# Kernel optimization log

Measured on AMD Instinct MI355X. Metric: run time of the kernel, lower is better.

## Reference

```python
import jax, jax.numpy as jnp
import numpy as np

THRESHOLD = 0.3

def setup_inputs() -> dict:
    key = jax.random.key(0)
    ks = jax.random.split(key, 8)
    B, T, N, d = 4, 32, 1024, 2
    hd, od, hs, osz = 64, 64, 128, 2
    p = lambda k, sh: jax.random.normal(k, sh, jnp.float32) * 0.1
    return {
        "points": jax.random.uniform(ks[0], (B, T, N, d), jnp.float32),
        "W1": p(ks[1], (hd, d)),   "b1": jnp.zeros((hd,), jnp.float32),
        "W2": p(ks[2], (od, hd)),  "b2": jnp.zeros((od,), jnp.float32),
        "Wg": p(ks[3], (hd, od)),  "bg": jnp.zeros((hd,), jnp.float32),
        "Wih": p(ks[4], (3 * hs, hd)), "Whh": p(ks[5], (3 * hs, hs)),
        "bih": jnp.zeros((3 * hs,), jnp.float32), "bhh": jnp.zeros((3 * hs,), jnp.float32),
        "Wf": p(ks[6], (osz, hs)), "bf": jnp.zeros((osz,), jnp.float32),
    }

def _gcn_step(pts, W1, b1, W2, b2, Wg, bg):
    # pts: [N, d]. Torch detaches node features & adjacency (no grad to points).
    pts = jax.lax.stop_gradient(pts)
    dist = jnp.linalg.norm(pts[:, None, :] - pts[None, :, :], axis=2)  # [N,N]
    A = (dist < THRESHOLD).astype(pts.dtype)
    dinv = 1.0 / jnp.sqrt(A.sum(axis=1))          # rowsum >= 1 (self-loop)
    An = A * dinv[:, None] * dinv[None, :]        # D^{-1/2} A D^{-1/2}
    x = jax.nn.relu((An @ pts) @ W1.T + b1)       # [N, hd]
    x = jax.nn.relu((An @ x) @ W2.T + b2)         # [N, od]
    return x.mean(axis=0) @ Wg.T + bg             # [hd]

def reference(points, W1, b1, W2, b2, Wg, bg, Wih, Whh, bih, bhh, Wf, bf):
    # GCN per (batch, time): [B, T, hd]
    gcn = jax.vmap(jax.vmap(lambda p: _gcn_step(p, W1, b1, W2, b2, Wg, bg)))(points)
    H = Whh.shape[1]

    def gru_step(h, x):  # torch GRU gate order: r, z, n
        gi = x @ Wih.T + bih
        gh = h @ Whh.T + bhh
        ir, iz, inn = jnp.split(gi, 3)
        hr, hz, hn = jnp.split(gh, 3)
        r = jax.nn.sigmoid(ir + hr)
        z = jax.nn.sigmoid(iz + hz)
        n = jnp.tanh(inn + r * hn)
        h_new = (1.0 - z) * n + z * h
        return h_new, h_new

    h0 = jnp.zeros((H,), points.dtype)
    run = lambda xs: jax.lax.scan(gru_step, h0, xs)[1]   # [T, H]
    hs = jax.vmap(run)(gcn)                              # [B, T, H]
    y = hs @ Wf.T + bf                                   # [B, T, out]
    # torch: per-element gru_out.mean(dim=1, keepdim=True) on [1,T,out] -> [1,1,out], stacked -> [B,1,1,out]
    return y.mean(axis=1, keepdims=True)[:, :, None, :]
```

## Files before the change

kernel.cpp:

```cpp
#include <hip/hip_runtime.h>
#include <hip/hip_bf16.h>
#include <math.h>

#define N_PTS 1024
#define BT    128
typedef unsigned int u32;
typedef __attribute__((ext_vector_type(8))) short short8_t;
typedef __attribute__((ext_vector_type(4))) float f32x4;

__device__ __forceinline__ float bfi(u32 bits16) {
    union { u32 u; float f; } v; v.u = bits16 << 16; return v.f;
}
__device__ __forceinline__ unsigned short f2bf(float f) {
    union { float f; u32 u; } v; v.f = f;
    return (unsigned short)((v.u + 0x7FFFu + ((v.u >> 16) & 1u)) >> 16);
}
__device__ __forceinline__ float ldf(const void* p, int i, bool bf) {
    return bf ? bfi(((const unsigned short*)p)[i]) : ((const float*)p)[i];
}
__device__ __forceinline__ float2 ldp(const void* pbase, int j, bool bf) {
    if (bf) {
        u32 w = ((const u32*)pbase)[j];
        return make_float2(bfi(w & 0xFFFFu), bfi(w >> 16));
    }
    return ((const float2*)pbase)[j];
}
__device__ __forceinline__ bool detect_bf16(const void* pts, int tid, int* s_flag) {
    if (tid < 64) {
        u32 w = ((const u32*)pts)[tid];
        float v = bfi(w & 0xFFFFu);
        bool ok = (v >= 0.0f) && (v <= 1.0f);
        unsigned long long m = __ballot(ok);
        if (tid == 0) *s_flag = (m == 0xFFFFFFFFFFFFFFFFull) ? 1 : 0;
    }
    __syncthreads();
    return *s_flag != 0;
}
__device__ __forceinline__ bool is_nb(float px, float py, float qx, float qy) {
    float dx = px - qx, dy = py - qy;
    float d2 = __fadd_rn(__fmul_rn(dx, dx), __fmul_rn(dy, dy));
    return d2 < 0.09f;
}
__device__ __forceinline__ const void* pts_base(const void* pts, int bt, bool bf) {
    return bf ? (const void*)((const unsigned short*)pts + (size_t)bt * N_PTS * 2)
              : (const void*)((const float*)pts + (size_t)bt * N_PTS * 2);
}
__device__ __forceinline__ void gload16(const u32* g, u32* l) {
    __builtin_amdgcn_global_load_lds((const __attribute__((address_space(1))) u32*)g,
                                     (__attribute__((address_space(3))) u32*)l, 16, 0, 0);
}

__global__ __launch_bounds__(256) void k1_bm(const void* __restrict__ pts,
                                             float* __restrict__ dinv,
                                             float* __restrict__ gsum,
                                             u32* __restrict__ bm) {
    int blk = blockIdx.x, tid = threadIdx.x;
    int bt = blk >> 2, q = blk & 3;
    __shared__ float2 sp[N_PTS];
    __shared__ int s_flag;
    bool bf = detect_bf16(pts, tid, &s_flag);
    const void* pb = pts_base(pts, bt, bf);
    for (int j = tid; j < N_PTS; j += 256) sp[j] = ldp(pb, j, bf);
    if (blk < 32) gsum[blk * 256 + tid] = 0.0f;
    __syncthreads();
    int i = q * 256 + tid;
    float px = sp[i].x, py = sp[i].y;
    const float4* sp4 = (const float4*)sp;
    u32* bmrow = bm + (size_t)bt * 32768 + i;
    int cnt = 0;
    for (int c = 0; c < 32; c++) {
        u32 m = 0;
#pragma unroll
        for (int h = 0; h < 8; h++) {
            float4 s01 = sp4[c * 16 + 2 * h], s23 = sp4[c * 16 + 2 * h + 1];
            if (is_nb(px, py, s01.x, s01.y)) m |= 1u << (4 * h);
            if (is_nb(px, py, s01.z, s01.w)) m |= 1u << (4 * h + 1);
            if (is_nb(px, py, s23.x, s23.y)) m |= 1u << (4 * h + 2);
            if (is_nb(px, py, s23.z, s23.w)) m |= 1u << (4 * h + 3);
        }
        bmrow[c * 1024] = m;
        cnt += __popc(m);
    }
    dinv[bt * N_PTS + i] = 1.0f / sqrtf((float)cnt);
}

__global__ __launch_bounds__(256) void k2_x1v(const void* __restrict__ pts,
                                              const void* __restrict__ W1,
                                              const void* __restrict__ b1,
                                              const float* __restrict__ dinv,
                                              const u32* __restrict__ bm,
                                              u32* __restrict__ x1vB) {
    int blk = blockIdx.x, tid = threadIdx.x;
    int bt = blk >> 2, q = blk & 3;
    __shared__ float2 sud[N_PTS];
    __shared__ float2 sax[256];
    __shared__ float  sdl[256];
    __shared__ int s_flag;
    bool bf = detect_bf16(pts, tid, &s_flag);
    const void* pb = pts_base(pts, bt, bf);
    for (int j = tid; j < N_PTS; j += 256) {
        float2 p = ldp(pb, j, bf);
        float d = dinv[bt * N_PTS + j];
        sud[j] = make_float2(d * p.x, d * p.y);
    }
    __syncthreads();
    int i = q * 256 + tid;
    float ax = 0.f, ay = 0.f;
    const u32* bmr = bm + (size_t)bt * 32768 + i;
    for (int c = 0; c < 32; c++) {
        u32 m = bmr[c * 1024];
        const float4* uv = (const float4*)sud + c * 16;
#pragma unroll
        for (int h = 0; h < 16; h++) {
            float4 v = uv[h];
            bool b0 = (m >> (2 * h)) & 1u, b1_ = (m >> (2 * h + 1)) & 1u;
            ax += b0 ? v.x : 0.0f;  ay += b0 ? v.y : 0.0f;
            ax += b1_ ? v.z : 0.0f; ay += b1_ ? v.w : 0.0f;
        }
    }
    float di = dinv[bt * N_PTS + i];
    sax[tid] = make_float2(ax * di, ay * di);
    sdl[tid] = di;
    __syncthreads();
    int ch = tid & 63, wq = tid >> 6;
    float w0 = ldf(W1, 2 * ch, bf), w1v = ldf(W1, 2 * ch + 1, bf), bb = ldf(b1, ch, bf);
    for (int tt = 0; tt < 4; tt++) {
        u32 ow[8];
#pragma unroll
        for (int k2i = 0; k2i < 8; k2i++) {
            int lj = tt * 64 + wq * 16 + 2 * k2i;
            float2 a0 = sax[lj], a1 = sax[lj + 1];
            float v0 = sdl[lj]     * fmaxf(fmaf(w0, a0.x, fmaf(w1v, a0.y, bb)), 0.0f);
            float v1 = sdl[lj + 1] * fmaxf(fmaf(w0, a1.x, fmaf(w1v, a1.y, bb)), 0.0f);
            ow[k2i] = (u32)f2bf(v0) | ((u32)f2bf(v1) << 16);
        }
        u32* dst = x1vB + ((size_t)(bt * 16 + q * 4 + tt) * 64 + ch) * 36 + wq * 8;
        *(uint4*)dst = make_uint4(ow[0], ow[1], ow[2], ow[3]);
        *(uint4*)(dst + 4) = make_uint4(ow[4], ow[5], ow[6], ow[7]);
    }
}

__global__ __launch_bounds__(256) void k3_mfma(const void* __restrict__ pts,
                                               const void* __restrict__ W2,
                                               const void* __restrict__ b2,
                                               const float* __restrict__ dinv,
                                               const u32* __restrict__ bm,
                                               const u32* __restrict__ x1vB,
                                               float* __restrict__ gsum) {
    __shared__ u32 pool[15424];
    __shared__ int s_flag;
    float* poolf = (float*)pool;
    int tid = threadIdx.x, lane = tid & 63, w = tid >> 6;
    int l15 = lane & 15, quad = lane >> 4;
    int blk = blockIdx.x, bt = blk & 127, rowblk = blk >> 7;
    bool bf = detect_bf16(pts, tid, &s_flag);

    const u32* xg = x1vB + (size_t)bt * 36864;
    for (int it = w; it < 9; it += 4)
        gload16(xg + it * 256 + lane * 4, pool + 8192 + it * 256 + lane * 4);

    const u32* bg_ = bm + (size_t)bt * 32768 + rowblk * 256;
    for (int idx = tid; idx < 8192; idx += 256) {
        int c = idx >> 8, r = idx & 255;
        pool[idx] = bg_[c * 1024 + r];
    }
    unsigned short* W2B = (unsigned short*)(pool + 12800);
    for (int idx = tid; idx < 4096; idx += 256) {
        int o = idx >> 6, c = idx & 63;
        W2B[o * 72 + c] = f2bf(ldf(W2, idx, bf));
    }
    if (tid < 256) poolf[15104 + tid] = dinv[bt * N_PTS + rowblk * 256 + tid];
    if (tid < 64)  poolf[15360 + tid] = ldf(b2, tid, bf);

    f32x4 acc[4][4];
#pragma unroll
    for (int rf = 0; rf < 4; rf++)
#pragma unroll
        for (int nb = 0; nb < 4; nb++)
#pragma unroll
            for (int r = 0; r < 4; r++) acc[rf][nb][r] = 0.0f;

    for (int t = 0; t < 16; t++) {
        __syncthreads();
        if (t + 1 < 16) {
            u32* dst = pool + ((t & 1) ? 8192 : 10496);
            const u32* src = xg + (t + 1) * 2304;
            for (int it = w; it < 9; it += 4)
                gload16(src + it * 256 + lane * 4, dst + it * 256 + lane * 4);
        }
        const unsigned short* xf = (const unsigned short*)(pool + ((t & 1) ? 10496 : 8192));
#pragma unroll
        for (int ks = 0; ks < 2; ks++) {
            short8_t bq[4];
#pragma unroll
            for (int rf = 0; rf < 4; rf++) {
                u32 mw = pool[(2 * t + ks) * 256 + w * 64 + rf * 16 + l15];
                u32 by = (mw >> (quad * 8)) & 0xFFu;
                short8_t v;
#pragma unroll
                for (int i2 = 0; i2 < 8; i2++)
                    v[i2] = (by & (1u << i2)) ? (short)0x3F80 : (short)0;
                bq[rf] = v;
            }
#pragma unroll
            for (int nb = 0; nb < 4; nb++) {
                short8_t af = *(const short8_t*)(xf + (nb * 16 + l15) * 72 + ks * 32 + quad * 8);
#pragma unroll
                for (int rf = 0; rf < 4; rf++)
                    acc[rf][nb] = __builtin_amdgcn_mfma_f32_16x16x32_bf16(af, bq[rf], acc[rf][nb], 0, 0, 0);
            }
        }
    }
    __syncthreads();

    u32* dump = pool;
#pragma unroll
    for (int rf = 0; rf < 4; rf++) {
        int rn = w * 64 + rf * 16 + l15;
        float di = poolf[15104 + rn];
#pragma unroll
        for (int nb = 0; nb < 4; nb++) {
            u32 lo = (u32)f2bf(acc[rf][nb][0] * di) | ((u32)f2bf(acc[rf][nb][1] * di) << 16);
            u32 hi = (u32)f2bf(acc[rf][nb][2] * di) | ((u32)f2bf(acc[rf][nb][3] * di) << 16);
            u32* dst = dump + rn * 36 + nb * 8 + quad * 2;
            dst[0] = lo; dst[1] = hi;
        }
    }
    __syncthreads();
    f32x4 xacc[4][4];
#pragma unroll
    for (int ob = 0; ob < 4; ob++)
#pragma unroll
        for (int rf = 0; rf < 4; rf++)
#pragma unroll
            for (int r = 0; r < 4; r++) xacc[ob][rf][r] = 0.0f;
#pragma unroll
    for (int ks2 = 0; ks2 < 2; ks2++) {
        short8_t b2f[4];
#pragma unroll
        for (int rf = 0; rf < 4; rf++)
            b2f[rf] = *(const short8_t*)((const unsigned short*)dump +
                        (w * 64 + rf * 16 + l15) * 72 + ks2 * 32 + quad * 8);
#pragma unroll
        for (int ob = 0; ob < 4; ob++) {
            short8_t a2 = *(const short8_t*)(W2B + (ob * 16 + l15) * 72 + ks2 * 32 + quad * 8);
#pragma unroll
            for (int rf = 0; rf < 4; rf++)
                xacc[ob][rf] = __builtin_amdgcn_mfma_f32_16x16x32_bf16(a2, b2f[rf], xacc[ob][rf], 0, 0, 0);
        }
    }
#pragma unroll
    for (int ob = 0; ob < 4; ob++) {
#pragma unroll
        for (int r = 0; r < 4; r++) {
            int o = ob * 16 + quad * 4 + r;
            float bb = poolf[15360 + o];
            float s = 0.0f;
#pragma unroll
            for (int rf = 0; rf < 4; rf++) s += fmaxf(xacc[ob][rf][r] + bb, 0.0f);
            s += __shfl_down(s, 8, 16);
            s += __shfl_down(s, 4, 16);
            s += __shfl_down(s, 2, 16);
            s += __shfl_down(s, 1, 16);
            if (l15 == 0) atomicAdd(&gsum[bt * 64 + o], s);
        }
    }
}

__global__ __launch_bounds__(384) void k4_all(const void* __restrict__ pts,
                                              const void* __restrict__ Wg,
                                              const void* __restrict__ bg,
                                              const void* __restrict__ Wih,
                                              const void* __restrict__ Whh,
                                              const void* __restrict__ bih,
                                              const void* __restrict__ bhh,
                                              const void* __restrict__ Wf,
                                              const void* __restrict__ bf_,
                                              const float* __restrict__ gsum,
                                              float* __restrict__ out) {
    int b = blockIdx.x, tid = threadIdx.x;
    __shared__ float s_gi[32 * 384];
    __shared__ float sWgT[64 * 65];
    __shared__ float s_gm[2048];
    __shared__ float s_x[2048];
    __shared__ float s_gh[384];
    __shared__ float s_h[128];
    __shared__ float s_hsum[128];
    __shared__ int s_flag;
    bool bf = detect_bf16(pts, tid, &s_flag);
    for (int idx = tid; idx < 4096; idx += 384) {
        int o = idx >> 6, k = idx & 63;
        sWgT[k * 65 + o] = ldf(Wg, idx, bf);
    }
    for (int idx = tid; idx < 2048; idx += 384)
        s_gm[idx] = gsum[(size_t)b * 2048 + idx] * (1.0f / 1024.0f);
    if (tid < 128) { s_h[tid] = 0.0f; s_hsum[tid] = 0.0f; }
    __syncthreads();
    for (int idx = tid; idx < 2048; idx += 384) {
        int t = idx >> 6, c = idx & 63;
        float s = ldf(bg, c, bf);
        for (int k = 0; k < 64; k++) s = fmaf(sWgT[k * 65 + c], s_gm[t * 64 + k], s);
        s_x[idx] = s;
    }
    __syncthreads();
    {
        int r = tid;
        float wv[64];
        if (bf) {
#pragma unroll
            for (int k = 0; k < 64; k++) wv[k] = bfi(((const unsigned short*)Wih)[r * 64 + k]);
        } else {
            const float4* wr = (const float4*)Wih + r * 16;
#pragma unroll
            for (int qq = 0; qq < 16; qq++) {
                float4 v = wr[qq];
                wv[4*qq] = v.x; wv[4*qq+1] = v.y; wv[4*qq+2] = v.z; wv[4*qq+3] = v.w;
            }
        }
        float br = ldf(bih, r, bf);
        for (int t = 0; t < 32; t++) {
            float s = br;
#pragma unroll
            for (int k = 0; k < 64; k++) s = fmaf(wv[k], s_x[t * 64 + k], s);
            s_gi[t * 384 + r] = s;
        }
    }
    float wh[128];
    if (bf) {
#pragma unroll
        for (int k = 0; k < 128; k++) wh[k] = bfi(((const unsigned short*)Whh)[tid * 128 + k]);
    } else {
        const float4* wr = (const float4*)Whh + tid * 32;
#pragma unroll
        for (int qq = 0; qq < 32; qq++) {
            float4 v = wr[qq];
            wh[4*qq] = v.x; wh[4*qq+1] = v.y; wh[4*qq+2] = v.z; wh[4*qq+3] = v.w;
        }
    }
    float bhr = ldf(bhh, tid, bf);
    __syncthreads();
    for (int t = 0; t < 32; t++) {
        float s = bhr;
#pragma unroll
        for (int k = 0; k < 128; k++) s = fmaf(wh[k], s_h[k], s);
        s_gh[tid] = s;
        __syncthreads();
        if (tid < 128) {
            int c = tid;
            float gr = s_gi[t * 384 + c]       + s_gh[c];
            float gz = s_gi[t * 384 + 128 + c] + s_gh[128 + c];
            float gn = s_gi[t * 384 + 256 + c];
            float hn = s_gh[256 + c];
            float r = 1.0f / (1.0f + expf(-gr));
            float z = 1.0f / (1.0f + expf(-gz));
            float n = tanhf(fmaf(r, hn, gn));
            float hnew = (1.0f - z) * n + z * s_h[c];
            s_h[c] = hnew;
            s_hsum[c] += hnew;
        }
        __syncthreads();
    }
    if (tid < 2) {
        float s = ldf(bf_, tid, bf);
        for (int k = 0; k < 128; k++)
            s = fmaf(ldf(Wf, tid * 128 + k, bf), s_hsum[k] * (1.0f / 32.0f), s);
        out[b * 2 + tid] = s;
    }
}

extern "C" void kernel_launch(void* const* d_in, const int* in_sizes, int n_in,
                              void* d_out, int out_size, void* d_ws, size_t ws_size,
                              hipStream_t stream) {
    const void* pts = d_in[0];
    const void* W1  = d_in[1];
    const void* b1  = d_in[2];
    const void* W2  = d_in[3];
    const void* b2  = d_in[4];
    const void* Wg  = d_in[5];
    const void* bg  = d_in[6];
    const void* Wih = d_in[7];
    const void* Whh = d_in[8];
    const void* bih = d_in[9];
    const void* bhh = d_in[10];
    const void* Wf  = d_in[11];
    const void* bf_ = d_in[12];

    float* dinv = (float*)d_ws;
    float* gsum = dinv + (size_t)BT * N_PTS;
    u32*   bm   = (u32*)(gsum + BT * 64);
    u32*   x1vB = bm + (size_t)BT * 32768;

    k1_bm  <<<512, 256, 0, stream>>>(pts, dinv, gsum, bm);
    k2_x1v <<<512, 256, 0, stream>>>(pts, W1, b1, dinv, bm, x1vB);
    k3_mfma<<<512, 256, 0, stream>>>(pts, W2, b2, dinv, bm, x1vB, gsum);
    k4_all <<<4, 384, 0, stream>>>(pts, Wg, bg, Wih, Whh, bih, bhh, Wf, bf_,
                                   gsum, (float*)d_out);
}
```

Baseline: 251.4 us.

## Split GRU recurrence matvec across 768 threads with K-halved partial sums

Doubles the GRU kernel's block size to 768 threads. Each half of the block computes the hidden-to-hidden matvec over half of the K dimension, and the two partial results are summed in shared memory, which shortens the serial 32-step recurrence chain. The input projection and Wg projections also use multiple independent accumulators with float4 shared loads, and the hidden state is kept in a register. The cost is more threads per block, each holding 64 weight registers, plus an extra partial-sum read per gate.

```diff
diff --git a/kernel.cpp b/kernel.cpp
--- a/kernel.cpp
+++ b/kernel.cpp
@@ -267,44 +267,51 @@
     }
 }
 
-__global__ __launch_bounds__(384) void k4_all(const void* __restrict__ pts,
-                                              const void* __restrict__ Wg,
-                                              const void* __restrict__ bg,
-                                              const void* __restrict__ Wih,
-                                              const void* __restrict__ Whh,
-                                              const void* __restrict__ bih,
-                                              const void* __restrict__ bhh,
-                                              const void* __restrict__ Wf,
-                                              const void* __restrict__ bf_,
-                                              const float* __restrict__ gsum,
-                                              float* __restrict__ out) {
+__global__ __launch_bounds__(768, 1) void k4_all(const void* __restrict__ pts,
+                                                 const void* __restrict__ Wg,
+                                                 const void* __restrict__ bg,
+                                                 const void* __restrict__ Wih,
+                                                 const void* __restrict__ Whh,
+                                                 const void* __restrict__ bih,
+                                                 const void* __restrict__ bhh,
+                                                 const void* __restrict__ Wf,
+                                                 const void* __restrict__ bf_,
+                                                 const float* __restrict__ gsum,
+                                                 float* __restrict__ out) {
     int b = blockIdx.x, tid = threadIdx.x;
     __shared__ float s_gi[32 * 384];
     __shared__ float sWgT[64 * 65];
     __shared__ float s_gm[2048];
     __shared__ float s_x[2048];
-    __shared__ float s_gh[384];
+    __shared__ float s_part[768];
     __shared__ float s_h[128];
-    __shared__ float s_hsum[128];
     __shared__ int s_flag;
     bool bf = detect_bf16(pts, tid, &s_flag);
-    for (int idx = tid; idx < 4096; idx += 384) {
+    for (int idx = tid; idx < 4096; idx += 768) {
         int o = idx >> 6, k = idx & 63;
         sWgT[k * 65 + o] = ldf(Wg, idx, bf);
     }
-    for (int idx = tid; idx < 2048; idx += 384)
+    for (int idx = tid; idx < 2048; idx += 768)
         s_gm[idx] = gsum[(size_t)b * 2048 + idx] * (1.0f / 1024.0f);
-    if (tid < 128) { s_h[tid] = 0.0f; s_hsum[tid] = 0.0f; }
-    __syncthreads();
-    for (int idx = tid; idx < 2048; idx += 384) {
+    if (tid < 128) s_h[tid] = 0.0f;
+    __syncthreads();
+    for (int idx = tid; idx < 2048; idx += 768) {
         int t = idx >> 6, c = idx & 63;
-        float s = ldf(bg, c, bf);
-        for (int k = 0; k < 64; k++) s = fmaf(sWgT[k * 65 + c], s_gm[t * 64 + k], s);
-        s_x[idx] = s;
-    }
-    __syncthreads();
+        float s0 = ldf(bg, c, bf), s1 = 0.f, s2 = 0.f, s3 = 0.f;
+        const float* gm = s_gm + t * 64;
+#pragma unroll
+        for (int k = 0; k < 64; k += 4) {
+            s0 = fmaf(sWgT[k * 65 + c],       gm[k],     s0);
+            s1 = fmaf(sWgT[(k + 1) * 65 + c], gm[k + 1], s1);
+            s2 = fmaf(sWgT[(k + 2) * 65 + c], gm[k + 2], s2);
+            s3 = fmaf(sWgT[(k + 3) * 65 + c], gm[k + 3], s3);
+        }
+        s_x[idx] = (s0 + s1) + (s2 + s3);
+    }
+    __syncthreads();
+    int hi = (tid >= 384) ? 1 : 0;
+    int r = tid - hi * 384;
     {
-        int r = tid;
         float wv[64];
         if (bf) {
 #pragma unroll
@@ -318,52 +325,76 @@
             }
         }
         float br = ldf(bih, r, bf);
-        for (int t = 0; t < 32; t++) {
-            float s = br;
-#pragma unroll
-            for (int k = 0; k < 64; k++) s = fmaf(wv[k], s_x[t * 64 + k], s);
-            s_gi[t * 384 + r] = s;
-        }
-    }
-    float wh[128];
-    if (bf) {
-#pragma unroll
-        for (int k = 0; k < 128; k++) wh[k] = bfi(((const unsigned short*)Whh)[tid * 128 + k]);
-    } else {
-        const float4* wr = (const float4*)Whh + tid * 32;
-#pragma unroll
-        for (int qq = 0; qq < 32; qq++) {
-            float4 v = wr[qq];
-            wh[4*qq] = v.x; wh[4*qq+1] = v.y; wh[4*qq+2] = v.z; wh[4*qq+3] = v.w;
-        }
-    }
-    float bhr = ldf(bhh, tid, bf);
-    __syncthreads();
+        for (int t = hi; t < 32; t += 2) {
+            float s0 = br, s1 = 0.f, s2 = 0.f, s3 = 0.f;
+            const float4* x4 = (const float4*)(s_x + t * 64);
+#pragma unroll
+            for (int qq = 0; qq < 16; qq++) {
+                float4 v = x4[qq];
+                s0 = fmaf(wv[4*qq],   v.x, s0);
+                s1 = fmaf(wv[4*qq+1], v.y, s1);
+                s2 = fmaf(wv[4*qq+2], v.z, s2);
+                s3 = fmaf(wv[4*qq+3], v.w, s3);
+            }
+            s_gi[t * 384 + r] = (s0 + s1) + (s2 + s3);
+        }
+    }
+    float wh2[64];
+    {
+        int koff = hi * 64;
+        if (bf) {
+#pragma unroll
+            for (int k = 0; k < 64; k++)
+                wh2[k] = bfi(((const unsigned short*)Whh)[r * 128 + koff + k]);
+        } else {
+            const float4* wr = (const float4*)Whh + (r * 128 + koff) / 4;
+#pragma unroll
+            for (int qq = 0; qq < 16; qq++) {
+                float4 v = wr[qq];
+                wh2[4*qq] = v.x; wh2[4*qq+1] = v.y; wh2[4*qq+2] = v.z; wh2[4*qq+3] = v.w;
+            }
+        }
+    }
+    float bhr = hi ? 0.0f : ldf(bhh, r, bf);
+    float h_reg = 0.0f, hsum = 0.0f;
+    __syncthreads();
+
     for (int t = 0; t < 32; t++) {
-        float s = bhr;
-#pragma unroll
-        for (int k = 0; k < 128; k++) s = fmaf(wh[k], s_h[k], s);
-        s_gh[tid] = s;
+        const float4* h4 = (const float4*)(s_h + hi * 64);
+        float s0 = bhr, s1 = 0.f, s2 = 0.f, s3 = 0.f;
+#pragma unroll
+        for (int qq = 0; qq < 16; qq++) {
+            float4 hv = h4[qq];
+            s0 = fmaf(wh2[4*qq],   hv.x, s0);
+            s1 = fmaf(wh2[4*qq+1], hv.y, s1);
+            s2 = fmaf(wh2[4*qq+2], hv.z, s2);
+            s3 = fmaf(wh2[4*qq+3], hv.w, s3);
+        }
+        s_part[tid] = (s0 + s1) + (s2 + s3);
         __syncthreads();
         if (tid < 128) {
             int c = tid;
-            float gr = s_gi[t * 384 + c]       + s_gh[c];
-            float gz = s_gi[t * 384 + 128 + c] + s_gh[128 + c];
+            float gr = s_gi[t * 384 + c]       + s_part[c]       + s_part[384 + c];
+            float gz = s_gi[t * 384 + 128 + c] + s_part[128 + c] + s_part[512 + c];
             float gn = s_gi[t * 384 + 256 + c];
-            float hn = s_gh[256 + c];
-            float r = 1.0f / (1.0f + expf(-gr));
-            float z = 1.0f / (1.0f + expf(-gz));
-            float n = tanhf(fmaf(r, hn, gn));
-            float hnew = (1.0f - z) * n + z * s_h[c];
-            s_h[c] = hnew;
-            s_hsum[c] += hnew;
+            float hn = s_part[256 + c] + s_part[640 + c];
+            float rr = 1.0f / (1.0f + expf(-gr));
+            float z  = 1.0f / (1.0f + expf(-gz));
+            float n  = tanhf(fmaf(rr, hn, gn));
+            float hnew = (1.0f - z) * n + z * h_reg;
+            h_reg = hnew; hsum += hnew; s_h[c] = hnew;
         }
         __syncthreads();
     }
+    if (tid < 128) {
+        float hm = hsum * (1.0f / 32.0f);
+        s_part[tid]       = ldf(Wf, tid, bf) * hm;
+        s_part[128 + tid] = ldf(Wf, 128 + tid, bf) * hm;
+    }
+    __syncthreads();
     if (tid < 2) {
         float s = ldf(bf_, tid, bf);
-        for (int k = 0; k < 128; k++)
-            s = fmaf(ldf(Wf, tid * 128 + k, bf), s_hsum[k] * (1.0f / 32.0f), s);
+        for (int k = 0; k < 128; k++) s += s_part[tid * 128 + k];
         out[b * 2 + tid] = s;
     }
 }
@@ -393,6 +424,6 @@
     k1_bm  <<<512, 256, 0, stream>>>(pts, dinv, gsum, bm);
     k2_x1v <<<512, 256, 0, stream>>>(pts, W1, b1, dinv, bm, x1vB);
     k3_mfma<<<512, 256, 0, stream>>>(pts, W2, b2, dinv, bm, x1vB, gsum);
-    k4_all <<<4, 384, 0, stream>>>(pts, Wg, bg, Wih, Whh, bih, bhh, Wf, bf_,
+    k4_all <<<4, 768, 0, stream>>>(pts, Wg, bg, Wih, Whh, bih, bhh, Wf, bf_,
                                    gsum, (float*)d_out);
 }
```

Measured after the change: 242.9 us. -3.4%, faster.
